# Kernel tuning notes

Measured on AMD Instinct MI355X. Metric: run time of the kernel, lower is better.

Reference implementation:

```python
import jax, jax.numpy as jnp
import numpy as np

B, S, E, H, L, V = 2, 2048, 512, 8, 4, 10000
D = E // H  # head_dim = 64


def _linear(x, W, b):
    # torch nn.Linear: y = x @ W.T + b, W: [out, in]
    return jnp.einsum('bse,oe->bso', x, W) + b


def _layernorm(x, g, b, eps=1e-5):
    mu = jnp.mean(x, axis=-1, keepdims=True)
    var = jnp.mean((x - mu) ** 2, axis=-1, keepdims=True)
    return (x - mu) * jax.lax.rsqrt(var + eps) * g + b


def _mha(x, Wq, bq, Wk, bk, Wv, bv, Wo, bo):
    q = _linear(x, Wq, bq).reshape(B, S, H, D).transpose(0, 2, 1, 3)
    k = _linear(x, Wk, bk).reshape(B, S, H, D).transpose(0, 2, 1, 3)
    v = _linear(x, Wv, bv).reshape(B, S, H, D).transpose(0, 2, 1, 3)
    energy = jnp.einsum('bhqd,bhkd->bhqk', q, k)  # full [B,H,S,S] scores (faithful)
    attn = jax.nn.softmax(energy / jnp.sqrt(jnp.asarray(D, x.dtype)), axis=-1)
    out = jnp.einsum('bhqk,bhkd->bhqd', attn, v)
    out = out.transpose(0, 2, 1, 3).reshape(B, S, E)
    return _linear(out, Wo, bo)


def setup_inputs() -> dict:
    key = jax.random.key(0)
    ks = jax.random.split(key, 12)
    s = 0.02
    f32 = jnp.float32
    return {
        'tokens': jax.random.randint(ks[0], (B, S), 0, V, dtype=jnp.int32),
        'embed_table': jax.random.normal(ks[1], (V, E), f32) * s,
        'pos_enc': jax.random.normal(ks[2], (1, S, E), f32) * s,
        'Wq': jax.random.normal(ks[3], (L, E, E), f32) * s,
        'bq': jnp.zeros((L, E), f32),
        'Wk': jax.random.normal(ks[4], (L, E, E), f32) * s,
        'bk': jnp.zeros((L, E), f32),
        'Wv': jax.random.normal(ks[5], (L, E, E), f32) * s,
        'bv': jnp.zeros((L, E), f32),
        'Wo': jax.random.normal(ks[6], (L, E, E), f32) * s,
        'bo': jnp.zeros((L, E), f32),
        'ln_g': jnp.ones((L, E), f32),
        'ln_b': jnp.zeros((L, E), f32),
        'Wout': jax.random.normal(ks[7], (V, E), f32) * s,
        'bout': jnp.zeros((V,), f32),
    }


def reference(tokens, embed_table, pos_enc, Wq, bq, Wk, bk, Wv, bv, Wo, bo, ln_g, ln_b, Wout, bout):
    x = embed_table[tokens] + pos_enc[:, :S, :]
    for l in range(L):
        a = _mha(x, Wq[l], bq[l], Wk[l], bk[l], Wv[l], bv[l], Wo[l], bo[l])
        x = _layernorm(x + a, ln_g[l], ln_b[l])
    # NOTE: original module defines feed_forward but never calls it in forward()
    return jnp.einsum('bse,ve->bsv', x, Wout) + bout
```

## Files before the change

kernel.cpp:

```cpp
#include <hip/hip_runtime.h>
#include <hip/hip_bf16.h>

#define Bc 2
#define Sc 2048
#define Ec 512
#define Hc 8
#define Lc 4
#define Vc 10000
#define Dc 64
#define Mc (Bc*Sc)
#define NPAD 10112
#define NROWS (16*Sc)

typedef __hip_bfloat16 bf16;
typedef __attribute__((ext_vector_type(8))) short frag_ab;
typedef __attribute__((ext_vector_type(4))) float frag_cd;

typedef __attribute__((address_space(3))) void lds_t;
typedef __attribute__((address_space(1))) void gm_t;
static __device__ __forceinline__ void gload16(const void* g, void* l) {
  __builtin_amdgcn_global_load_lds((const gm_t*)g, (lds_t*)l, 16, 0, 0);
}
static __device__ __forceinline__ frag_ab ldfrag(const bf16* p) {
  return *(const frag_ab*)p;
}

#define ROR16(x, n) __uint_as_float((unsigned)__builtin_amdgcn_update_dpp( \
    0, (int)__float_as_uint(x), 0x120 | (n), 0xf, 0xf, true))
static __device__ __forceinline__ float rmax16(float x) {
  x = fmaxf(x, ROR16(x, 8));
  x = fmaxf(x, ROR16(x, 4));
  x = fmaxf(x, ROR16(x, 2));
  x = fmaxf(x, ROR16(x, 1));
  return x;
}
static __device__ __forceinline__ float rsum16(float x) {
  x += ROR16(x, 8);
  x += ROR16(x, 4);
  x += ROR16(x, 2);
  x += ROR16(x, 1);
  return x;
}

#define NQKV (Lc*1536*512)
#define NO   (Lc*512*512)
#define NOUT (NPAD*512)
__global__ void convert_kernel(const float* __restrict__ Wq, const float* __restrict__ Wk,
                               const float* __restrict__ Wv, const float* __restrict__ Wo,
                               const float* __restrict__ Wout,
                               bf16* __restrict__ wqkv, bf16* __restrict__ wo,
                               bf16* __restrict__ wout) {
  long i4 = (long)(blockIdx.x * 256 + threadIdx.x) * 4;
  if (i4 >= NQKV + NO + NOUT) return;
  float4 v;
  bf16* dst;
  if (i4 < NQKV) {
    int row = (int)(i4 >> 9), colb = (int)(i4 & 511);
    int l = row / 1536, rr = row - l * 1536;
    int seg = rr >> 9, r = rr & 511;
    const float* src = (seg == 0 ? Wq : seg == 1 ? Wk : Wv) + (((long)(l * 512 + r)) << 9) + colb;
    v = *(const float4*)src;
    dst = wqkv + i4;
  } else if (i4 < NQKV + NO) {
    long j = i4 - NQKV;
    v = *(const float4*)(Wo + j);
    dst = wo + j;
  } else {
    long j = i4 - NQKV - NO;
    int row = (int)(j >> 9);
    if (row < Vc) v = *(const float4*)(Wout + j);
    else { v.x = 0.f; v.y = 0.f; v.z = 0.f; v.w = 0.f; }
    dst = wout + j;
  }
  union { bf16 h[4]; short4 s4; } u;
  u.h[0] = __float2bfloat16(v.x);
  u.h[1] = __float2bfloat16(v.y);
  u.h[2] = __float2bfloat16(v.z);
  u.h[3] = __float2bfloat16(v.w);
  *(short4*)dst = u.s4;
}

__global__ void embed_kernel(const int* __restrict__ tok, const float* __restrict__ emb,
                             const float* __restrict__ pos, float* __restrict__ x,
                             bf16* __restrict__ xb) {
  int i = blockIdx.x * 256 + threadIdx.x;
  int row = i >> 9, c = i & 511;
  int s = row & (Sc - 1);
  float v = emb[tok[row] * Ec + c] + pos[s * Ec + c];
  x[i] = v;
  xb[i] = __float2bfloat16(v);
}

template<int MODE>
__global__ __launch_bounds__(256)
void gemm_tile(const bf16* __restrict__ A, const bf16* __restrict__ W,
               const float* __restrict__ b0, const float* __restrict__ b1,
               const float* __restrict__ b2,
               void* __restrict__ o0, void* __restrict__ o1, void* __restrict__ o2) {
  __shared__ bf16 As[128 * 32];
  __shared__ bf16 Bs[128 * 32];
  const int t = threadIdx.x;
  const int lane = t & 63;
  const int wv = t >> 6;
  const int c = lane & 15, quad = lane >> 4;
  const int m0 = blockIdx.x * 128, n0 = blockIdx.y * 128;
  const int wm = (wv & 1) * 64, wn = (wv >> 1) * 64;
  frag_cd acc[4][4] = {};

  const int p0 = t, p1 = t + 256;
  const int r0 = p0 >> 2, g0 = (p0 & 3) ^ ((r0 >> 1) & 3);
  const int r1 = p1 >> 2, g1 = (p1 & 3) ^ ((r1 >> 1) & 3);
  const bf16* a0 = A + (m0 + r0) * Ec + g0 * 8;
  const bf16* a1 = A + (m0 + r1) * Ec + g1 * 8;
  const bf16* w0 = W + (n0 + r0) * Ec + g0 * 8;
  const bf16* w1 = W + (n0 + r1) * Ec + g1 * 8;

  const int sw8 = ((quad ^ ((c >> 1) & 3))) * 8;

  for (int k = 0; k < Ec; k += 32) {
    __syncthreads();
    gload16(a0 + k, As + p0 * 8);
    gload16(a1 + k, As + p1 * 8);
    gload16(w0 + k, Bs + p0 * 8);
    gload16(w1 + k, Bs + p1 * 8);
    __syncthreads();
    frag_ab af[4], bfr[4];
#pragma unroll
    for (int i = 0; i < 4; ++i)
      af[i] = *(const frag_ab*)(As + (wm + i * 16 + c) * 32 + sw8);
#pragma unroll
    for (int j = 0; j < 4; ++j)
      bfr[j] = *(const frag_ab*)(Bs + (wn + j * 16 + c) * 32 + sw8);
#pragma unroll
    for (int i = 0; i < 4; ++i)
#pragma unroll
      for (int j = 0; j < 4; ++j)
        acc[i][j] = __builtin_amdgcn_mfma_f32_16x16x32_bf16(af[i], bfr[j], acc[i][j], 0, 0, 0);
  }

#pragma unroll
  for (int j = 0; j < 4; ++j) {
    int gn = n0 + wn + j * 16 + c;
    if (MODE == 0) {
      int seg = gn >> 9, col = gn & 511;
      const float* bp = seg == 0 ? b0 : seg == 1 ? b1 : b2;
      float bias = bp[col];
      int hh = col >> 6, dd = col & 63;
#pragma unroll
      for (int i = 0; i < 4; ++i)
#pragma unroll
        for (int ii = 0; ii < 4; ++ii) {
          int gm = m0 + wm + i * 16 + quad * 4 + ii;
          int bb = gm >> 11, ss = gm & (Sc - 1);
          float v = acc[i][j][ii] + bias;
          if (seg == 0)
            ((bf16*)o0)[((((bb << 3) + hh) * Sc + ss) << 6) + dd] = __float2bfloat16(v);
          else if (seg == 1)
            ((bf16*)o1)[((((bb << 3) + hh) * Sc + ss) << 6) + dd] = __float2bfloat16(v);
          else
            ((bf16*)o2)[((((bb << 3) + hh) << 6) + dd) * Sc + ss] = __float2bfloat16(v);
        }
    } else if (MODE == 1) {
      float bias = b0[gn];
#pragma unroll
      for (int i = 0; i < 4; ++i)
#pragma unroll
        for (int ii = 0; ii < 4; ++ii) {
          int gm = m0 + wm + i * 16 + quad * 4 + ii;
          ((float*)o0)[((long)gm << 9) + gn] = acc[i][j][ii] + bias;
        }
    } else {
      if (gn < Vc) {
        float bias = b0[gn];
#pragma unroll
        for (int i = 0; i < 4; ++i)
#pragma unroll
          for (int ii = 0; ii < 4; ++ii) {
            int gm = m0 + wm + i * 16 + quad * 4 + ii;
            ((float*)o0)[(long)gm * Vc + gn] = acc[i][j][ii] + bias;
          }
      }
    }
  }
}

__global__ __launch_bounds__(256, 2)
void attn_kernel(const bf16* __restrict__ Q, const bf16* __restrict__ Kb,
                 const bf16* __restrict__ Vt,
                 float* __restrict__ Op, float* __restrict__ mp, float* __restrict__ lp) {
  __shared__ bf16 Ks[2][64 * 64];
  __shared__ bf16 Vs[2][64 * 64];
  __shared__ bf16 Ps[4][2][16 * 64];
  const int t = threadIdx.x;
  const int lane = t & 63, wv = t >> 6;
  const int c = lane & 15, quad = lane >> 4;

  int wg = (blockIdx.x & 7) * 64 + (blockIdx.x >> 3);
  const int bh = wg >> 5;
  const int split = (wg >> 4) & 1;
  const int q0 = (wg & 15) * 128 + wv * 32;

  const bf16* kbase = Kb + (long)bh * Sc * Dc + (long)(split << 10) * Dc;
  const bf16* vbase = Vt + (long)bh * Dc * Sc + (split << 10);

  const int p0 = t, p1 = t + 256;
  const int row0 = (p0 >> 2) & 63, g40 = (p0 & 3) ^ ((row0 >> 1) & 3);
  const int row1 = (p1 >> 2) & 63, g41 = (p1 & 3) ^ ((row1 >> 1) & 3);
  const bf16* ksrc0 = kbase + row0 * Dc + 0 * 32 + g40 * 8;
  const bf16* ksrc1 = kbase + row1 * Dc + 1 * 32 + g41 * 8;
  const bf16* vsrc0 = vbase + row0 * Sc + 0 * 32 + g40 * 8;
  const bf16* vsrc1 = vbase + row1 * Sc + 1 * 32 + g41 * 8;

  const bf16* qpA = Q + ((long)bh * Sc + q0 + c) * Dc + quad * 8;
  frag_ab aq0A = ldfrag(qpA);
  frag_ab aq1A = ldfrag(qpA + 32);
  const bf16* qpB = qpA + 16 * Dc;
  frag_ab aq0B = ldfrag(qpB);
  frag_ab aq1B = ldfrag(qpB + 32);

  const int sw8 = (quad ^ ((c >> 1) & 3)) * 8;

  float mA[4], lAr[4], mB[4], lBr[4];
  frag_cd oA[4] = {}, oB[4] = {};
#pragma unroll
  for (int i = 0; i < 4; ++i) { mA[i] = -1e30f; mB[i] = -1e30f; lAr[i] = 0.f; lBr[i] = 0.f; }

  bf16* plA = Ps[wv][0];
  bf16* plB = Ps[wv][1];

  gload16(ksrc0, Ks[0] + p0 * 8);
  gload16(ksrc1, Ks[0] + p1 * 8);
  gload16(vsrc0, Vs[0] + p0 * 8);
  gload16(vsrc1, Vs[0] + p1 * 8);

  for (int tI = 0; tI < 16; ++tI) {
    const int cur = tI & 1;
    if (tI < 15) {
      const int k0 = (tI + 1) * 64;
      bf16* kd = Ks[cur ^ 1];
      bf16* vd = Vs[cur ^ 1];
      gload16(ksrc0 + k0 * Dc, kd + p0 * 8);
      gload16(ksrc1 + k0 * Dc, kd + p1 * 8);
      gload16(vsrc0 + k0, vd + p0 * 8);
      gload16(vsrc1 + k0, vd + p1 * 8);
      asm volatile("s_waitcnt vmcnt(4)" ::: "memory");
    } else {
      asm volatile("s_waitcnt vmcnt(0)" ::: "memory");
    }
    __builtin_amdgcn_s_barrier();
    asm volatile("" ::: "memory");

    const bf16* KsB = Ks[cur];
    const bf16* VsB = Vs[cur];

    frag_cd sA[4] = {}, sB[4] = {};
#pragma unroll
    for (int j = 0; j < 4; ++j) {
      frag_ab kb0 = ldfrag(KsB + (j * 16 + c) * 32 + sw8);
      frag_ab kb1 = ldfrag(KsB + 2048 + (j * 16 + c) * 32 + sw8);
      sA[j] = __builtin_amdgcn_mfma_f32_16x16x32_bf16(aq0A, kb0, sA[j], 0, 0, 0);
      sA[j] = __builtin_amdgcn_mfma_f32_16x16x32_bf16(aq1A, kb1, sA[j], 0, 0, 0);
      sB[j] = __builtin_amdgcn_mfma_f32_16x16x32_bf16(aq0B, kb0, sB[j], 0, 0, 0);
      sB[j] = __builtin_amdgcn_mfma_f32_16x16x32_bf16(aq1B, kb1, sB[j], 0, 0, 0);
    }

    float alA[4], alB[4];
#pragma unroll
    for (int i = 0; i < 4; ++i) {
      float sc0 = sA[0][i] * 0.125f, sc1 = sA[1][i] * 0.125f;
      float sc2 = sA[2][i] * 0.125f, sc3 = sA[3][i] * 0.125f;
      float mx = rmax16(fmaxf(fmaxf(sc0, sc1), fmaxf(sc2, sc3)));
      float mn = fmaxf(mA[i], mx);
      alA[i] = __expf(mA[i] - mn);
      float pe0 = __expf(sc0 - mn), pe1 = __expf(sc1 - mn);
      float pe2 = __expf(sc2 - mn), pe3 = __expf(sc3 - mn);
      float rs = rsum16(pe0 + pe1 + pe2 + pe3);
      lAr[i] = lAr[i] * alA[i] + rs;
      mA[i] = mn;
      int row = quad * 4 + i;
      plA[row * 64 + ((((c >> 3) + 0) ^ (row & 7)) << 3) + (c & 7)] = __float2bfloat16(pe0);
      plA[row * 64 + ((((c >> 3) + 2) ^ (row & 7)) << 3) + (c & 7)] = __float2bfloat16(pe1);
      plA[row * 64 + ((((c >> 3) + 4) ^ (row & 7)) << 3) + (c & 7)] = __float2bfloat16(pe2);
      plA[row * 64 + ((((c >> 3) + 6) ^ (row & 7)) << 3) + (c & 7)] = __float2bfloat16(pe3);
    }
#pragma unroll
    for (int i = 0; i < 4; ++i) {
      float sc0 = sB[0][i] * 0.125f, sc1 = sB[1][i] * 0.125f;
      float sc2 = sB[2][i] * 0.125f, sc3 = sB[3][i] * 0.125f;
      float mx = rmax16(fmaxf(fmaxf(sc0, sc1), fmaxf(sc2, sc3)));
      float mn = fmaxf(mB[i], mx);
      alB[i] = __expf(mB[i] - mn);
      float pe0 = __expf(sc0 - mn), pe1 = __expf(sc1 - mn);
      float pe2 = __expf(sc2 - mn), pe3 = __expf(sc3 - mn);
      float rs = rsum16(pe0 + pe1 + pe2 + pe3);
      lBr[i] = lBr[i] * alB[i] + rs;
      mB[i] = mn;
      int row = quad * 4 + i;
      plB[row * 64 + ((((c >> 3) + 0) ^ (row & 7)) << 3) + (c & 7)] = __float2bfloat16(pe0);
      plB[row * 64 + ((((c >> 3) + 2) ^ (row & 7)) << 3) + (c & 7)] = __float2bfloat16(pe1);
      plB[row * 64 + ((((c >> 3) + 4) ^ (row & 7)) << 3) + (c & 7)] = __float2bfloat16(pe2);
      plB[row * 64 + ((((c >> 3) + 6) ^ (row & 7)) << 3) + (c & 7)] = __float2bfloat16(pe3);
    }

#pragma unroll
    for (int td = 0; td < 4; ++td)
#pragma unroll
      for (int i = 0; i < 4; ++i) { oA[td][i] *= alA[i]; oB[td][i] *= alB[i]; }
#pragma unroll
    for (int kk = 0; kk < 2; ++kk) {
      frag_ab apA = ldfrag(plA + c * 64 + ((((kk << 2) + quad) ^ (c & 7)) << 3));
      frag_ab apB = ldfrag(plB + c * 64 + ((((kk << 2) + quad) ^ (c & 7)) << 3));
#pragma unroll
      for (int td = 0; td < 4; ++td) {
        frag_ab vb = ldfrag(VsB + kk * 2048 + (td * 16 + c) * 32 + sw8);
        oA[td] = __builtin_amdgcn_mfma_f32_16x16x32_bf16(apA, vb, oA[td], 0, 0, 0);
        oB[td] = __builtin_amdgcn_mfma_f32_16x16x32_bf16(apB, vb, oB[td], 0, 0, 0);
      }
    }

    asm volatile("" ::: "memory");
    __builtin_amdgcn_s_barrier();
  }

  const long rbase = (long)split * NROWS + (long)bh * Sc + q0;
#pragma unroll
  for (int i = 0; i < 4; ++i) {
    long rA = rbase + quad * 4 + i;
    long rB = rA + 16;
    if (c == 0) {
      mp[rA] = mA[i]; lp[rA] = lAr[i];
      mp[rB] = mB[i]; lp[rB] = lBr[i];
    }
#pragma unroll
    for (int td = 0; td < 4; ++td) {
      Op[rA * Dc + td * 16 + c] = oA[td][i];
      Op[rB * Dc + td * 16 + c] = oB[td][i];
    }
  }
}

__global__ void combine_kernel(const float* __restrict__ Op, const float* __restrict__ mp,
                               const float* __restrict__ lp, bf16* __restrict__ O) {
  int t = blockIdx.x * 256 + threadIdx.x;
  int d = t & 63, r = t >> 6;
  int bh = r >> 11, ss = r & (Sc - 1);
  float m1 = mp[r], m2 = mp[NROWS + r];
  float l1 = lp[r], l2 = lp[NROWS + r];
  float M = fmaxf(m1, m2);
  float a1 = __expf(m1 - M), a2 = __expf(m2 - M);
  float denom = l1 * a1 + l2 * a2;
  float o = (Op[(long)r * Dc + d] * a1 + Op[(long)(NROWS + r) * Dc + d] * a2) / denom;
  int bb = bh >> 3, hh = bh & 7;
  O[((long)bb * Sc + ss) * Ec + hh * Dc + d] = __float2bfloat16(o);
}

__global__ void ln_kernel(const float* __restrict__ x, const float* __restrict__ a,
                          const float* __restrict__ g, const float* __restrict__ bb,
                          float* __restrict__ xo, bf16* __restrict__ xbo) {
  int lane = threadIdx.x & 63, wv = threadIdx.x >> 6;
  int row = blockIdx.x * 4 + wv;
  const float* xr = x + (long)row * Ec;
  const float* ar = a + (long)row * Ec;
  float v[8];
  float sum = 0.f;
#pragma unroll
  for (int j = 0; j < 8; ++j) {
    int c = lane + j * 64;
    v[j] = xr[c] + ar[c];
    sum += v[j];
  }
#pragma unroll
  for (int d = 1; d < 64; d <<= 1) sum += __shfl_xor(sum, d, 64);
  float mu = sum * (1.f / 512.f);
  float sq = 0.f;
#pragma unroll
  for (int j = 0; j < 8; ++j) { float t = v[j] - mu; sq += t * t; }
#pragma unroll
  for (int d = 1; d < 64; d <<= 1) sq += __shfl_xor(sq, d, 64);
  float rs = 1.f / sqrtf(sq * (1.f / 512.f) + 1e-5f);
#pragma unroll
  for (int j = 0; j < 8; ++j) {
    int c = lane + j * 64;
    float y = (v[j] - mu) * rs * g[c] + bb[c];
    xo[(long)row * Ec + c] = y;
    xbo[(long)row * Ec + c] = __float2bfloat16(y);
  }
}

extern "C" void kernel_launch(void* const* d_in, const int* in_sizes, int n_in,
                              void* d_out, int out_size, void* d_ws, size_t ws_size,
                              hipStream_t stream) {
  const int*   tokens = (const int*)d_in[0];
  const float* embed  = (const float*)d_in[1];
  const float* pos    = (const float*)d_in[2];
  const float* Wq     = (const float*)d_in[3];
  const float* bq     = (const float*)d_in[4];
  const float* Wk     = (const float*)d_in[5];
  const float* bk     = (const float*)d_in[6];
  const float* Wv     = (const float*)d_in[7];
  const float* bv     = (const float*)d_in[8];
  const float* Wo     = (const float*)d_in[9];
  const float* bo     = (const float*)d_in[10];
  const float* ln_g   = (const float*)d_in[11];
  const float* ln_b   = (const float*)d_in[12];
  const float* Wout   = (const float*)d_in[13];
  const float* bout   = (const float*)d_in[14];
  float* out = (float*)d_out;

  char* ws = (char*)d_ws;
  size_t off = 0;
  float* x_f    = (float*)(ws + off); off += (size_t)Mc * Ec * 4;
  bf16*  xb     = (bf16*)(ws + off);  off += (size_t)Mc * Ec * 2;
  float* a_f    = (float*)(ws + off); off += (size_t)Mc * Ec * 4;
  bf16*  qb     = (bf16*)(ws + off);  off += (size_t)Mc * Ec * 2;
  bf16*  kb     = (bf16*)(ws + off);  off += (size_t)Mc * Ec * 2;
  bf16*  vtb    = (bf16*)(ws + off);  off += (size_t)Mc * Ec * 2;
  bf16*  attnb  = (bf16*)(ws + off);  off += (size_t)Mc * Ec * 2;
  bf16*  wqkv_b = (bf16*)(ws + off);  off += (size_t)NQKV * 2;
  bf16*  wo_b   = (bf16*)(ws + off);  off += (size_t)NO * 2;
  bf16*  wout_b = (bf16*)(ws + off);  off += (size_t)NOUT * 2;
  float* op_f   = (float*)(ws + off); off += (size_t)2 * NROWS * Dc * 4;
  float* mp_f   = (float*)(ws + off); off += (size_t)2 * NROWS * 4;
  float* lp_f   = (float*)(ws + off); off += (size_t)2 * NROWS * 4;

  int nconv = (NQKV + NO + NOUT) / 4;
  convert_kernel<<<(nconv + 255) / 256, 256, 0, stream>>>(Wq, Wk, Wv, Wo, Wout,
                                                          wqkv_b, wo_b, wout_b);

  embed_kernel<<<(Mc * Ec) / 256, 256, 0, stream>>>(tokens, embed, pos, x_f, xb);

  dim3 gqkv(Mc / 128, 1536 / 128);
  dim3 go(Mc / 128, Ec / 128);
  for (int l = 0; l < Lc; ++l) {
    const bf16* wqkv_l = wqkv_b + (size_t)l * 1536 * Ec;
    const bf16* wo_l   = wo_b + (size_t)l * Ec * Ec;
    gemm_tile<0><<<gqkv, 256, 0, stream>>>(xb, wqkv_l, bq + l * Ec, bk + l * Ec,
                                           bv + l * Ec, qb, kb, vtb);
    attn_kernel<<<2 * Hc * Bc * (Sc / 128), 256, 0, stream>>>(qb, kb, vtb,
                                                              op_f, mp_f, lp_f);
    combine_kernel<<<(NROWS * Dc) / 256, 256, 0, stream>>>(op_f, mp_f, lp_f, attnb);
    gemm_tile<1><<<go, 256, 0, stream>>>(attnb, wo_l, bo + l * Ec, nullptr, nullptr,
                                         a_f, nullptr, nullptr);
    ln_kernel<<<Mc / 4, 256, 0, stream>>>(x_f, a_f, ln_g + l * Ec, ln_b + l * Ec,
                                          x_f, xb);
  }

  dim3 glog(Mc / 128, NPAD / 128);
  gemm_tile<2><<<glog, 256, 0, stream>>>(xb, wout_b, bout, nullptr, nullptr,
                                         out, nullptr, nullptr);
}
```

Measured before the change: 663.1 us.

## Split attention KV into four chunks with lazy softmax rescaling via exp2

The attention kernel now splits each head's key/value range four ways instead of two, doubling the number of workgroups and raising the occupancy target in launch bounds. Scores are pre-scaled by log2(e)/sqrt(D) so exp2 replaces exp, and the running max and output rescale are only updated when some row's new max exceeds the stored one by more than 8 (checked by a wave ballot). The combine kernel merges four partials and processes two output elements per thread with packed bf16 stores. The extra splits add partial-output traffic and a larger combine step, and the lazy rescaling lets unnormalized exponentials grow up to 2^8 before renormalization.

```diff
diff --git a/kernel.cpp b/kernel.cpp
--- a/kernel.cpp
+++ b/kernel.cpp
@@ -11,6 +11,7 @@
 #define Mc (Bc*Sc)
 #define NPAD 10112
 #define NROWS (16*Sc)
+#define SPLITS 4
 
 typedef __hip_bfloat16 bf16;
 typedef __attribute__((ext_vector_type(8))) short frag_ab;
@@ -41,6 +42,8 @@
   x += ROR16(x, 1);
   return x;
 }
+
+#define SCALE2 0.18033688011112042f
 
 #define NQKV (Lc*1536*512)
 #define NO   (Lc*512*512)
@@ -184,7 +187,7 @@
   }
 }
 
-__global__ __launch_bounds__(256, 2)
+__global__ __launch_bounds__(256, 3)
 void attn_kernel(const bf16* __restrict__ Q, const bf16* __restrict__ Kb,
                  const bf16* __restrict__ Vt,
                  float* __restrict__ Op, float* __restrict__ mp, float* __restrict__ lp) {
@@ -195,13 +198,13 @@
   const int lane = t & 63, wv = t >> 6;
   const int c = lane & 15, quad = lane >> 4;
 
-  int wg = (blockIdx.x & 7) * 64 + (blockIdx.x >> 3);
-  const int bh = wg >> 5;
-  const int split = (wg >> 4) & 1;
+  int wg = (blockIdx.x & 7) * 128 + (blockIdx.x >> 3);
+  const int bh = wg >> 6;
+  const int split = (wg >> 4) & 3;
   const int q0 = (wg & 15) * 128 + wv * 32;
 
-  const bf16* kbase = Kb + (long)bh * Sc * Dc + (long)(split << 10) * Dc;
-  const bf16* vbase = Vt + (long)bh * Dc * Sc + (split << 10);
+  const bf16* kbase = Kb + (long)bh * Sc * Dc + (long)(split << 9) * Dc;
+  const bf16* vbase = Vt + (long)bh * Dc * Sc + (split << 9);
 
   const int p0 = t, p1 = t + 256;
   const int row0 = (p0 >> 2) & 63, g40 = (p0 & 3) ^ ((row0 >> 1) & 3);
@@ -233,9 +236,9 @@
   gload16(vsrc0, Vs[0] + p0 * 8);
   gload16(vsrc1, Vs[0] + p1 * 8);
 
-  for (int tI = 0; tI < 16; ++tI) {
+  for (int tI = 0; tI < 8; ++tI) {
     const int cur = tI & 1;
-    if (tI < 15) {
+    if (tI < 7) {
       const int k0 = (tI + 1) * 64;
       bf16* kd = Ks[cur ^ 1];
       bf16* vd = Vs[cur ^ 1];
@@ -264,19 +267,39 @@
       sB[j] = __builtin_amdgcn_mfma_f32_16x16x32_bf16(aq1B, kb1, sB[j], 0, 0, 0);
     }
 
+#pragma unroll
+    for (int j = 0; j < 4; ++j)
+#pragma unroll
+      for (int i = 0; i < 4; ++i) { sA[j][i] *= SCALE2; sB[j][i] *= SCALE2; }
+
+    float mxA[4], mxB[4];
+    bool needl = false;
+#pragma unroll
+    for (int i = 0; i < 4; ++i) {
+      mxA[i] = rmax16(fmaxf(fmaxf(sA[0][i], sA[1][i]), fmaxf(sA[2][i], sA[3][i])));
+      mxB[i] = rmax16(fmaxf(fmaxf(sB[0][i], sB[1][i]), fmaxf(sB[2][i], sB[3][i])));
+      needl |= (mxA[i] > mA[i] + 8.0f) | (mxB[i] > mB[i] + 8.0f);
+    }
+    const bool resc = (__ballot(needl) != 0ull);
     float alA[4], alB[4];
+    if (resc) {
+#pragma unroll
+      for (int i = 0; i < 4; ++i) {
+        float mnA = fmaxf(mA[i], mxA[i]);
+        float mnB = fmaxf(mB[i], mxB[i]);
+        alA[i] = exp2f(mA[i] - mnA);
+        alB[i] = exp2f(mB[i] - mnB);
+        mA[i] = mnA;
+        mB[i] = mnB;
+      }
+    }
+
 #pragma unroll
     for (int i = 0; i < 4; ++i) {
-      float sc0 = sA[0][i] * 0.125f, sc1 = sA[1][i] * 0.125f;
-      float sc2 = sA[2][i] * 0.125f, sc3 = sA[3][i] * 0.125f;
-      float mx = rmax16(fmaxf(fmaxf(sc0, sc1), fmaxf(sc2, sc3)));
-      float mn = fmaxf(mA[i], mx);
-      alA[i] = __expf(mA[i] - mn);
-      float pe0 = __expf(sc0 - mn), pe1 = __expf(sc1 - mn);
-      float pe2 = __expf(sc2 - mn), pe3 = __expf(sc3 - mn);
+      float pe0 = exp2f(sA[0][i] - mA[i]), pe1 = exp2f(sA[1][i] - mA[i]);
+      float pe2 = exp2f(sA[2][i] - mA[i]), pe3 = exp2f(sA[3][i] - mA[i]);
       float rs = rsum16(pe0 + pe1 + pe2 + pe3);
-      lAr[i] = lAr[i] * alA[i] + rs;
-      mA[i] = mn;
+      lAr[i] = resc ? lAr[i] * alA[i] + rs : lAr[i] + rs;
       int row = quad * 4 + i;
       plA[row * 64 + ((((c >> 3) + 0) ^ (row & 7)) << 3) + (c & 7)] = __float2bfloat16(pe0);
       plA[row * 64 + ((((c >> 3) + 2) ^ (row & 7)) << 3) + (c & 7)] = __float2bfloat16(pe1);
@@ -285,16 +308,10 @@
     }
 #pragma unroll
     for (int i = 0; i < 4; ++i) {
-      float sc0 = sB[0][i] * 0.125f, sc1 = sB[1][i] * 0.125f;
-      float sc2 = sB[2][i] * 0.125f, sc3 = sB[3][i] * 0.125f;
-      float mx = rmax16(fmaxf(fmaxf(sc0, sc1), fmaxf(sc2, sc3)));
-      float mn = fmaxf(mB[i], mx);
-      alB[i] = __expf(mB[i] - mn);
-      float pe0 = __expf(sc0 - mn), pe1 = __expf(sc1 - mn);
-      float pe2 = __expf(sc2 - mn), pe3 = __expf(sc3 - mn);
+      float pe0 = exp2f(sB[0][i] - mB[i]), pe1 = exp2f(sB[1][i] - mB[i]);
+      float pe2 = exp2f(sB[2][i] - mB[i]), pe3 = exp2f(sB[3][i] - mB[i]);
       float rs = rsum16(pe0 + pe1 + pe2 + pe3);
-      lBr[i] = lBr[i] * alB[i] + rs;
-      mB[i] = mn;
+      lBr[i] = resc ? lBr[i] * alB[i] + rs : lBr[i] + rs;
       int row = quad * 4 + i;
       plB[row * 64 + ((((c >> 3) + 0) ^ (row & 7)) << 3) + (c & 7)] = __float2bfloat16(pe0);
       plB[row * 64 + ((((c >> 3) + 2) ^ (row & 7)) << 3) + (c & 7)] = __float2bfloat16(pe1);
@@ -302,10 +319,12 @@
       plB[row * 64 + ((((c >> 3) + 6) ^ (row & 7)) << 3) + (c & 7)] = __float2bfloat16(pe3);
     }
 
-#pragma unroll
-    for (int td = 0; td < 4; ++td)
-#pragma unroll
-      for (int i = 0; i < 4; ++i) { oA[td][i] *= alA[i]; oB[td][i] *= alB[i]; }
+    if (resc) {
+#pragma unroll
+      for (int td = 0; td < 4; ++td)
+#pragma unroll
+        for (int i = 0; i < 4; ++i) { oA[td][i] *= alA[i]; oB[td][i] *= alB[i]; }
+    }
 #pragma unroll
     for (int kk = 0; kk < 2; ++kk) {
       frag_ab apA = ldfrag(plA + c * 64 + ((((kk << 2) + quad) ^ (c & 7)) << 3));
@@ -342,16 +361,31 @@
 __global__ void combine_kernel(const float* __restrict__ Op, const float* __restrict__ mp,
                                const float* __restrict__ lp, bf16* __restrict__ O) {
   int t = blockIdx.x * 256 + threadIdx.x;
-  int d = t & 63, r = t >> 6;
+  int d = (t & 31) * 2, r = t >> 5;
   int bh = r >> 11, ss = r & (Sc - 1);
-  float m1 = mp[r], m2 = mp[NROWS + r];
-  float l1 = lp[r], l2 = lp[NROWS + r];
-  float M = fmaxf(m1, m2);
-  float a1 = __expf(m1 - M), a2 = __expf(m2 - M);
-  float denom = l1 * a1 + l2 * a2;
-  float o = (Op[(long)r * Dc + d] * a1 + Op[(long)(NROWS + r) * Dc + d] * a2) / denom;
+  float ms[SPLITS], ls[SPLITS];
+  float M = -1e30f;
+#pragma unroll
+  for (int s = 0; s < SPLITS; ++s) {
+    ms[s] = mp[s * NROWS + r];
+    ls[s] = lp[s * NROWS + r];
+    M = fmaxf(M, ms[s]);
+  }
+  float denom = 0.f, o0 = 0.f, o1 = 0.f;
+#pragma unroll
+  for (int s = 0; s < SPLITS; ++s) {
+    float a = exp2f(ms[s] - M);
+    denom += ls[s] * a;
+    float2 v = *(const float2*)(Op + ((long)s * NROWS + r) * Dc + d);
+    o0 += v.x * a;
+    o1 += v.y * a;
+  }
+  float inv = 1.f / denom;
+  union { bf16 h[2]; unsigned u; } u2;
+  u2.h[0] = __float2bfloat16(o0 * inv);
+  u2.h[1] = __float2bfloat16(o1 * inv);
   int bb = bh >> 3, hh = bh & 7;
-  O[((long)bb * Sc + ss) * Ec + hh * Dc + d] = __float2bfloat16(o);
+  *(unsigned*)&O[((long)bb * Sc + ss) * Ec + hh * Dc + d] = u2.u;
 }
 
 __global__ void ln_kernel(const float* __restrict__ x, const float* __restrict__ a,
@@ -419,9 +453,9 @@
   bf16*  wqkv_b = (bf16*)(ws + off);  off += (size_t)NQKV * 2;
   bf16*  wo_b   = (bf16*)(ws + off);  off += (size_t)NO * 2;
   bf16*  wout_b = (bf16*)(ws + off);  off += (size_t)NOUT * 2;
-  float* op_f   = (float*)(ws + off); off += (size_t)2 * NROWS * Dc * 4;
-  float* mp_f   = (float*)(ws + off); off += (size_t)2 * NROWS * 4;
-  float* lp_f   = (float*)(ws + off); off += (size_t)2 * NROWS * 4;
+  float* op_f   = (float*)(ws + off); off += (size_t)SPLITS * NROWS * Dc * 4;
+  float* mp_f   = (float*)(ws + off); off += (size_t)SPLITS * NROWS * 4;
+  float* lp_f   = (float*)(ws + off); off += (size_t)SPLITS * NROWS * 4;
 
   int nconv = (NQKV + NO + NOUT) / 4;
   convert_kernel<<<(nconv + 255) / 256, 256, 0, stream>>>(Wq, Wk, Wv, Wo, Wout,
@@ -436,9 +470,9 @@
     const bf16* wo_l   = wo_b + (size_t)l * Ec * Ec;
     gemm_tile<0><<<gqkv, 256, 0, stream>>>(xb, wqkv_l, bq + l * Ec, bk + l * Ec,
                                            bv + l * Ec, qb, kb, vtb);
-    attn_kernel<<<2 * Hc * Bc * (Sc / 128), 256, 0, stream>>>(qb, kb, vtb,
-                                                              op_f, mp_f, lp_f);
-    combine_kernel<<<(NROWS * Dc) / 256, 256, 0, stream>>>(op_f, mp_f, lp_f, attnb);
+    attn_kernel<<<SPLITS * Hc * Bc * (Sc / 128), 256, 0, stream>>>(qb, kb, vtb,
+                                                                   op_f, mp_f, lp_f);
+    combine_kernel<<<(NROWS * 32) / 256, 256, 0, stream>>>(op_f, mp_f, lp_f, attnb);
     gemm_tile<1><<<go, 256, 0, stream>>>(attnb, wo_l, bo + l * Ec, nullptr, nullptr,
                                          a_f, nullptr, nullptr);
     ln_kernel<<<Mc / 4, 256, 0, stream>>>(x_f, a_f, ln_g + l * Ec, ln_b + l * Ec,
```

After: 691.4 us. 4.3% more time.
